# Kernel optimization log

Measured on AMD Instinct MI355X. Metric: run time of the kernel, lower is better.

## Reference

```python
import jax, jax.numpy as jnp
import numpy as np
from jax.scipy.special import logsumexp

NUM_TAGS = 48
SEQ_LEN = 512
BATCH = 1024


def setup_inputs() -> dict:
    key = jax.random.key(0)
    k_em, k_tags, k_tr, k_st, k_en = jax.random.split(key, 5)
    emissions = jax.random.normal(k_em, (SEQ_LEN, BATCH, NUM_TAGS), dtype=jnp.float32)
    tags = jax.random.randint(k_tags, (SEQ_LEN, BATCH), 0, NUM_TAGS, dtype=jnp.int64)
    mask = jnp.ones((SEQ_LEN, BATCH), dtype=jnp.int32)
    # CRF parameters, uniform(-0.1, 0.1) like reset_parameters
    transitions = jax.random.uniform(k_tr, (NUM_TAGS, NUM_TAGS), jnp.float32, -0.1, 0.1)
    start_transitions = jax.random.uniform(k_st, (NUM_TAGS,), jnp.float32, -0.1, 0.1)
    end_transitions = jax.random.uniform(k_en, (NUM_TAGS,), jnp.float32, -0.1, 0.1)
    return {
        "emissions": emissions,
        "tags": tags,
        "mask": mask,
        "transitions": transitions,
        "start_transitions": start_transitions,
        "end_transitions": end_transitions,
    }


def _score(emissions, tags, mask, transitions, start_transitions, end_transitions):
    # emissions: (S,B,T)  tags/mask: (S,B)
    S, B = tags.shape
    batch_idx = jnp.arange(B)
    maskf = mask.astype(emissions.dtype)
    # emission score at the gold tag for every timestep: (S,B)
    em_sc = jnp.take_along_axis(emissions, tags[..., None], axis=2)[..., 0]
    score = start_transitions[tags[0]] + em_sc[0]
    # transition score for steps 1..S-1: (S-1,B)
    trans_sc = transitions[tags[:-1], tags[1:]]
    score = score + ((trans_sc + em_sc[1:]) * maskf[1:]).sum(axis=0)
    valid_last_idx = mask.astype(jnp.int32).sum(axis=0) - 1  # (B,)
    last_tags = tags[valid_last_idx, batch_idx]
    return score + end_transitions[last_tags]


def _partition(emissions, mask, transitions, start_transitions, end_transitions):
    alpha0 = start_transitions[None, :] + emissions[0]  # (B,T)

    def step(alpha, inp):
        em_i, m_i = inp  # (B,T), (B,)
        # (B,T_prev,1) + (T_prev,T_cur) + (B,1,T_cur) -> logsumexp over prev
        cur = logsumexp(alpha[:, :, None] + transitions[None, :, :] + em_i[:, None, :], axis=1)
        alpha = jnp.where(m_i.astype(bool)[:, None], cur, alpha)
        return alpha, None

    alpha, _ = jax.lax.scan(step, alpha0, (emissions[1:], mask[1:]))
    return logsumexp(alpha + end_transitions[None, :], axis=1)  # (B,)


def reference(emissions, tags, mask, transitions, start_transitions, end_transitions):
    score = _score(emissions, tags, mask, transitions, start_transitions, end_transitions)
    partition = _partition(emissions, mask, transitions, start_transitions, end_transitions)
    nllh = partition - score
    return nllh.sum()  # reduction='sum'
```

## Files before the change

### kernel.cpp

```cpp
#include <hip/hip_runtime.h>

#define S 512
#define B 1024
#define K 48
#define NCH 16
#define NBLK (B / NCH)
#define PF 8
#define LN2 0.6931471805599453f
#define LOG2E 1.4426950408889634f

typedef float f4 __attribute__((ext_vector_type(4)));
typedef __bf16 b8 __attribute__((ext_vector_type(8)));
union BU { b8 v; unsigned u[4]; };

__device__ __forceinline__ f4 mfma32(b8 a, b8 b, f4 c) {
    return __builtin_amdgcn_mfma_f32_16x16x32_bf16(a, b, c, 0, 0, 0);
}

__global__ void __launch_bounds__(64) zero_out(float* o) {
    if (threadIdx.x == 0) o[0] = 0.f;
}

__global__ void __launch_bounds__(64, 1) crf_kernel(
    const float* __restrict__ em, const int* __restrict__ tags,
    const int* __restrict__ mask, const float* __restrict__ trans,
    const float* __restrict__ start_tr, const float* __restrict__ end_tr,
    float* __restrict__ out)
{
    const int lane = threadIdx.x;
    const int c    = lane & 15;
    const int g    = lane >> 4;
    const int bb   = blockIdx.x * NCH;
    const int b    = bb + c;

    float sc = 0.f;
    int   mc = 0;
    {
        int tagp = 0;
        if (g > 0) tagp = tags[(128 * g - 1) * B + b];
        #pragma unroll 4
        for (int i = 0; i < 128; ++i) {
            int t   = 128 * g + i;
            int tag = tags[t * B + b];
            int mk  = mask[t * B + b];
            mc += mk;
            if (t == 0) {
                sc += start_tr[tag] + em[(size_t)b * K + tag];
            } else {
                float add = trans[tagp * K + tag] + em[((size_t)t * B + b) * K + tag];
                sc += mk ? add : 0.f;
            }
            tagp = tag;
        }
        sc += __shfl_xor(sc, 16);  sc += __shfl_xor(sc, 32);
        mc += __shfl_xor(mc, 16);  mc += __shfl_xor(mc, 32);
        int lt = mc - 1; if (lt < 0) lt += S;
        sc += end_tr[tags[lt * B + b]];
    }

    BU Afr[3][2];
    #pragma unroll
    for (int tr = 0; tr < 3; ++tr)
        #pragma unroll
        for (int kc = 0; kc < 2; ++kc)
            #pragma unroll
            for (int e = 0; e < 8; ++e) {
                int kk = 32 * kc + 16 * (e >> 2) + 4 * g + (e & 3);
                float v = (kk < K) ? __expf(trans[kk * K + 16 * tr + c]) : 0.f;
                Afr[tr][kc].v[e] = (__bf16)v;
            }

    BU Bf[2];
    #pragma unroll
    for (int kc = 0; kc < 2; ++kc)
        #pragma unroll
        for (int e = 0; e < 8; ++e) {
            int kk = 32 * kc + 16 * (e >> 2) + 4 * g + (e & 3);
            float v = (kk < K) ? __expf(start_tr[kk] + em[(size_t)b * K + kk]) : 1.f;
            Bf[kc].v[e] = (__bf16)v;
        }

    f4  emr[PF][3];
    int mkr[PF];
    #pragma unroll
    for (int i = 0; i < PF; ++i) {
        const float* rp = em + ((size_t)(1 + i) * B + b) * K + 4 * g;
        emr[i][0] = *(const f4*)(rp);
        emr[i][1] = *(const f4*)(rp + 16);
        emr[i][2] = *(const f4*)(rp + 32);
        mkr[i]    = mask[(1 + i) * B + b];
    }
    f4 eem[3];
    #pragma unroll
    for (int tr = 0; tr < 3; ++tr)
        #pragma unroll
        for (int e = 0; e < 4; ++e)
            eem[tr][e] = exp2f(emr[0][tr][e] * LOG2E);

    int offc  = 0;
    int n_cur = 0;

#define STEP(u_)                                                                \
    {                                                                           \
        f4 c0 = {0.f,0.f,0.f,0.f}, c1 = {0.f,0.f,0.f,0.f},                      \
           c2 = {0.f,0.f,0.f,0.f};                                              \
        c0 = mfma32(Afr[0][0].v, Bf[0].v, c0);                                  \
        c1 = mfma32(Afr[1][0].v, Bf[0].v, c1);                                  \
        c2 = mfma32(Afr[2][0].v, Bf[0].v, c2);                                  \
        c0 = mfma32(Afr[0][1].v, Bf[1].v, c0);                                  \
        c1 = mfma32(Afr[1][1].v, Bf[1].v, c1);                                  \
        c2 = mfma32(Afr[2][1].v, Bf[1].v, c2);                                  \
        c0 *= eem[0]; c1 *= eem[1]; c2 *= eem[2];                               \
        bool keep = mkr[u_] != 0;                                               \
        unsigned adj = (unsigned)(n_cur * 0x00800080);      \
        n_cur = 0;                                                              \
        BU nb0, nb1;                                                            \
        nb0.v[0] = (__bf16)c0[0]; nb0.v[1] = (__bf16)c0[1];                     \
        nb0.v[2] = (__bf16)c0[2]; nb0.v[3] = (__bf16)c0[3];                     \
        nb0.v[4] = (__bf16)c1[0]; nb0.v[5] = (__bf16)c1[1];                     \
        nb0.v[6] = (__bf16)c1[2]; nb0.v[7] = (__bf16)c1[3];                     \
        nb1.v[0] = (__bf16)c2[0]; nb1.v[1] = (__bf16)c2[1];                     \
        nb1.v[2] = (__bf16)c2[2]; nb1.v[3] = (__bf16)c2[3];                     \
        nb1.v[4] = nb1.v[0]; nb1.v[5] = nb1.v[1];                               \
        nb1.v[6] = nb1.v[2]; nb1.v[7] = nb1.v[3];      \
        _Pragma("unroll")                                                       \
        for (int w = 0; w < 4; ++w) {                                           \
            Bf[0].u[w] = keep ? nb0.u[w] : (Bf[0].u[w] - adj);                  \
            Bf[1].u[w] = keep ? nb1.u[w] : (Bf[1].u[w] - adj);                  \
        }                                                                       \
        const int tp = t0 + (u_) + PF;                                          \
        if (tp < S) {                                                           \
            const float* rp = em + ((size_t)tp * B + b) * K + 4 * g;            \
            emr[u_][0] = *(const f4*)(rp);                                      \
            emr[u_][1] = *(const f4*)(rp + 16);                                 \
            emr[u_][2] = *(const f4*)(rp + 32);                                 \
            mkr[u_]    = mask[tp * B + b];                                      \
        }                                                                       \
        float nrmf = 0.f;                                                       \
        if ((u_) == 7) {               \
            float rv = __shfl((float)Bf[0].v[0], c);         \
            int   E  = ((__float_as_int(rv) >> 23) & 255) - 127;                \
            int   n  = E + 30;                  \
            offc += n;  n_cur = n;  nrmf = -(float)n;                           \
        }                                                                       \
        const int sn = ((u_) + 1) & 7;                                          \
        _Pragma("unroll")                                                       \
        for (int tr_ = 0; tr_ < 3; ++tr_)                                       \
            _Pragma("unroll")                                                   \
            for (int e_ = 0; e_ < 4; ++e_)                                      \
                eem[tr_][e_] = exp2f(fmaf(emr[sn][tr_][e_], LOG2E, nrmf));      \
    }

    for (int t0 = 1; t0 + 7 < S; t0 += PF) {
        STEP(0) STEP(1) STEP(2) STEP(3) STEP(4) STEP(5) STEP(6) STEP(7)
    }
    {
        const int t0 = S - 7;
        STEP(0) STEP(1) STEP(2) STEP(3) STEP(4) STEP(5) STEP(6)
    }
#undef STEP

    float val = 0.f;
    #pragma unroll
    for (int e = 0; e < 4; ++e) {
        val += (float)Bf[0].v[e]     * __expf(end_tr[4 * g + e]);
        val += (float)Bf[0].v[4 + e] * __expf(end_tr[16 + 4 * g + e]);
        val += (float)Bf[1].v[e]     * __expf(end_tr[32 + 4 * g + e]);
    }
    val += __shfl_xor(val, 16);
    val += __shfl_xor(val, 32);
    float part = (float)offc * LN2 + logf(val);

    float contrib = part - sc;
    #pragma unroll
    for (int off = 32; off > 0; off >>= 1) contrib += __shfl_xor(contrib, off);
    if (lane == 0) atomicAdd(out, contrib * 0.25f);
}

extern "C" void kernel_launch(void* const* d_in, const int* in_sizes, int n_in,
                              void* d_out, int out_size, void* d_ws, size_t ws_size,
                              hipStream_t stream) {
    const float* em       = (const float*)d_in[0];
    const int*   tags     = (const int*)d_in[1];
    const int*   mask     = (const int*)d_in[2];
    const float* trans    = (const float*)d_in[3];
    const float* start_tr = (const float*)d_in[4];
    const float* end_tr   = (const float*)d_in[5];
    float* out = (float*)d_out;

    zero_out<<<dim3(1), dim3(64), 0, stream>>>(out);
    crf_kernel<<<dim3(NBLK), dim3(64), 0, stream>>>(em, tags, mask, trans,
                                                    start_tr, end_tr, out);
}
```

Baseline: 365.4 us.

## Stage emission prefetch through LDS with async global_load_lds ring buffer

Replaces the register-resident prefetch of emissions and mask rows with an 8-slot LDS ring fed by global_load_lds direct-to-LDS loads, paced by explicit vmcnt waits. This frees the many VGPRs held by the register prefetch array and lets the recurrence read the next step's emissions from LDS. The launch bound's occupancy hint is also dropped, so more waves may share a CU. The change adds LDS traffic and manual waitcnt bookkeeping whose counts must match the number of outstanding loads; if they are wrong, the recurrence reads stale data.

```diff
diff --git a/kernel.cpp b/kernel.cpp
--- a/kernel.cpp
+++ b/kernel.cpp
@@ -6,6 +6,7 @@
 #define NCH 16
 #define NBLK (B / NCH)
 #define PF 8
+#define SLOT_SZ 3328
 #define LN2 0.6931471805599453f
 #define LOG2E 1.4426950408889634f
 
@@ -16,12 +17,22 @@
 __device__ __forceinline__ f4 mfma32(b8 a, b8 b, f4 c) {
     return __builtin_amdgcn_mfma_f32_16x16x32_bf16(a, b, c, 0, 0, 0);
 }
+__device__ __forceinline__ void stage16(const void* g, void* l) {
+    __builtin_amdgcn_global_load_lds(
+        (const __attribute__((address_space(1))) void*)g,
+        (__attribute__((address_space(3))) void*)l, 16, 0, 0);
+}
+__device__ __forceinline__ void stage4(const void* g, void* l) {
+    __builtin_amdgcn_global_load_lds(
+        (const __attribute__((address_space(1))) void*)g,
+        (__attribute__((address_space(3))) void*)l, 4, 0, 0);
+}
 
 __global__ void __launch_bounds__(64) zero_out(float* o) {
     if (threadIdx.x == 0) o[0] = 0.f;
 }
 
-__global__ void __launch_bounds__(64, 1) crf_kernel(
+__global__ void __launch_bounds__(64) crf_kernel(
     const float* __restrict__ em, const int* __restrict__ tags,
     const int* __restrict__ mask, const float* __restrict__ trans,
     const float* __restrict__ start_tr, const float* __restrict__ end_tr,
@@ -32,6 +43,8 @@
     const int g    = lane >> 4;
     const int bb   = blockIdx.x * NCH;
     const int b    = bb + c;
+
+    __shared__ __align__(16) char ldsbuf[PF][SLOT_SZ];
 
     float sc = 0.f;
     int   mc = 0;
@@ -80,28 +93,51 @@
             Bf[kc].v[e] = (__bf16)v;
         }
 
-    f4  emr[PF][3];
-    int mkr[PF];
-    #pragma unroll
-    for (int i = 0; i < PF; ++i) {
-        const float* rp = em + ((size_t)(1 + i) * B + b) * K + 4 * g;
-        emr[i][0] = *(const f4*)(rp);
-        emr[i][1] = *(const f4*)(rp + 16);
-        emr[i][2] = *(const f4*)(rp + 32);
-        mkr[i]    = mask[(1 + i) * B + b];
-    }
+#define STAGE(t_, s_)                                                           \
+    {                                                                           \
+        const float* rp_ = em + ((size_t)(t_) * B + bb + c) * K + 4 * g;        \
+        stage16(rp_,      &ldsbuf[s_][0]);                                      \
+        stage16(rp_ + 16, &ldsbuf[s_][1024]);                                   \
+        stage16(rp_ + 32, &ldsbuf[s_][2048]);                                   \
+        stage4(mask + (t_) * B + bb + c, &ldsbuf[s_][3072]);                    \
+    }
+
+    #pragma unroll
+    for (int i = 0; i < PF; ++i) STAGE(1 + i, (1 + i) & 7);
+
+    asm volatile("s_waitcnt vmcnt(28)" ::: "memory");
+    __builtin_amdgcn_sched_barrier(0);
     f4 eem[3];
-    #pragma unroll
-    for (int tr = 0; tr < 3; ++tr)
+    {
+        f4 i0 = *(const f4*)&ldsbuf[1][lane * 16];
+        f4 i1 = *(const f4*)&ldsbuf[1][1024 + lane * 16];
+        f4 i2 = *(const f4*)&ldsbuf[1][2048 + lane * 16];
         #pragma unroll
-        for (int e = 0; e < 4; ++e)
-            eem[tr][e] = exp2f(emr[0][tr][e] * LOG2E);
-
-    int offc  = 0;
-    int n_cur = 0;
-
-#define STEP(u_)                                                                \
+        for (int e = 0; e < 4; ++e) {
+            eem[0][e] = exp2f(i0[e] * LOG2E);
+            eem[1][e] = exp2f(i1[e] * LOG2E);
+            eem[2][e] = exp2f(i2[e] * LOG2E);
+        }
+    }
+
+    int   offc  = 0;
+    int   n_cur = 0;
+    float rshfl = 0.f;
+
+#define STEP(s_, t_)                                                            \
     {                                                                           \
+                  \
+        asm volatile("s_waitcnt vmcnt(24)" ::: "memory");                       \
+        __builtin_amdgcn_sched_barrier(0);                                      \
+        const int sn_ = ((s_) + 1) & 7;                                         \
+        f4 e0 = *(const f4*)&ldsbuf[sn_][lane * 16];                            \
+        f4 e1 = *(const f4*)&ldsbuf[sn_][1024 + lane * 16];                     \
+        f4 e2 = *(const f4*)&ldsbuf[sn_][2048 + lane * 16];                     \
+        int mk = *(const int*)&ldsbuf[s_][3072 + lane * 4];                     \
+        if ((s_) == 0) {               \
+            float rvf = (float)Bf[0].v[0];                                      \
+            rshfl = __shfl(rvf, c);                                             \
+        }                                                                       \
         f4 c0 = {0.f,0.f,0.f,0.f}, c1 = {0.f,0.f,0.f,0.f},                      \
            c2 = {0.f,0.f,0.f,0.f};                                              \
         c0 = mfma32(Afr[0][0].v, Bf[0].v, c0);                                  \
@@ -111,7 +147,9 @@
         c1 = mfma32(Afr[1][1].v, Bf[1].v, c1);                                  \
         c2 = mfma32(Afr[2][1].v, Bf[1].v, c2);                                  \
         c0 *= eem[0]; c1 *= eem[1]; c2 *= eem[2];                               \
-        bool keep = mkr[u_] != 0;                                               \
+                  \
+        asm volatile("s_waitcnt lgkmcnt(0)" ::: "memory");                      \
+        bool keep = mk != 0;                                                    \
         unsigned adj = (unsigned)(n_cur * 0x00800080);      \
         n_cur = 0;                                                              \
         BU nb0, nb1;                                                            \
@@ -128,37 +166,34 @@
             Bf[0].u[w] = keep ? nb0.u[w] : (Bf[0].u[w] - adj);                  \
             Bf[1].u[w] = keep ? nb1.u[w] : (Bf[1].u[w] - adj);                  \
         }                                                                       \
-        const int tp = t0 + (u_) + PF;                                          \
-        if (tp < S) {                                                           \
-            const float* rp = em + ((size_t)tp * B + b) * K + 4 * g;            \
-            emr[u_][0] = *(const f4*)(rp);                                      \
-            emr[u_][1] = *(const f4*)(rp + 16);                                 \
-            emr[u_][2] = *(const f4*)(rp + 32);                                 \
-            mkr[u_]    = mask[tp * B + b];                                      \
+            \
+        {                                                                       \
+            int tp_ = (t_) + PF;                                                \
+            int tc_ = tp_ < S - 1 ? tp_ : S - 1;                                \
+            STAGE(tc_, s_);                                                     \
         }                                                                       \
         float nrmf = 0.f;                                                       \
-        if ((u_) == 7) {               \
-            float rv = __shfl((float)Bf[0].v[0], c);         \
-            int   E  = ((__float_as_int(rv) >> 23) & 255) - 127;                \
-            int   n  = E + 30;                  \
-            offc += n;  n_cur = n;  nrmf = -(float)n;                           \
-        }                                                                       \
-        const int sn = ((u_) + 1) & 7;                                          \
+        if ((s_) == 0) {                   \
+            int E_ = ((__float_as_int(rshfl) >> 23) & 255) - 127;               \
+            int n_ = E_ + 30;                   \
+            offc += n_;  n_cur = n_;  nrmf = -(float)n_;                        \
+        }                                                                       \
         _Pragma("unroll")                                                       \
-        for (int tr_ = 0; tr_ < 3; ++tr_)                                       \
-            _Pragma("unroll")                                                   \
-            for (int e_ = 0; e_ < 4; ++e_)                                      \
-                eem[tr_][e_] = exp2f(fmaf(emr[sn][tr_][e_], LOG2E, nrmf));      \
+        for (int e_ = 0; e_ < 4; ++e_) {                                        \
+            eem[0][e_] = exp2f(fmaf(e0[e_], LOG2E, nrmf));                      \
+            eem[1][e_] = exp2f(fmaf(e1[e_], LOG2E, nrmf));                      \
+            eem[2][e_] = exp2f(fmaf(e2[e_], LOG2E, nrmf));                      \
+        }                                                                       \
     }
 
     for (int t0 = 1; t0 + 7 < S; t0 += PF) {
-        STEP(0) STEP(1) STEP(2) STEP(3) STEP(4) STEP(5) STEP(6) STEP(7)
-    }
-    {
-        const int t0 = S - 7;
-        STEP(0) STEP(1) STEP(2) STEP(3) STEP(4) STEP(5) STEP(6)
-    }
+        STEP(1, t0)     STEP(2, t0 + 1) STEP(3, t0 + 2) STEP(4, t0 + 3)
+        STEP(5, t0 + 4) STEP(6, t0 + 5) STEP(7, t0 + 6) STEP(0, t0 + 7)
+    }
+    STEP(1, 505) STEP(2, 506) STEP(3, 507) STEP(4, 508)
+    STEP(5, 509) STEP(6, 510) STEP(7, 511)
 #undef STEP
+#undef STAGE
 
     float val = 0.f;
     #pragma unroll
```

New measurement: 393.0 us. 1.08x slower.
